# Optimization experiments

Measured on AMD Instinct MI355X. Metric: run time of the kernel, lower is better.

The kernel has to match this reference:

```python
import jax, jax.numpy as jnp
import numpy as np

NQ = 4      # n_qubits
NL = 1      # n_layers
IN_DIM = 512
HIDDEN = 256
B = 131072


def _apply_1q(state, gate, q, batched):
    """Apply a single-qubit gate on qubit q. state: [B, 2**NQ] complex.
    gate: [2,2] (shared) or [B,2,2] (per-sample)."""
    Bsz = state.shape[0]
    left, right = 2 ** q, 2 ** (NQ - q - 1)
    s = state.reshape(Bsz, left, 2, right)
    if batched:
        s = jnp.einsum('bij,bljr->blir', gate, s)
    else:
        s = jnp.einsum('ij,bljr->blir', gate, s)
    return s.reshape(Bsz, -1)


def _cnot_adjacent(state, q):
    """CNOT with control q, target q+1 (adjacent wires only)."""
    Bsz = state.shape[0]
    left, right = 2 ** q, 2 ** (NQ - q - 2)
    s = state.reshape(Bsz, left, 2, 2, right)
    # control=0 branch unchanged; control=1 branch has target flipped
    s = jnp.stack([s[:, :, 0], s[:, :, 1, ::-1]], axis=2)
    return s.reshape(Bsz, -1)


def _rot_gate(phi, theta, omega):
    """PennyLane Rot(phi,theta,omega) = RZ(omega) RY(theta) RZ(phi)."""
    c, s = jnp.cos(theta / 2), jnp.sin(theta / 2)
    ep = jnp.exp(-0.5j * (phi + omega).astype(jnp.complex64))
    em = jnp.exp(-0.5j * (phi - omega).astype(jnp.complex64))
    return jnp.array([[1.0, 0.0], [0.0, 0.0]], jnp.complex64) * (ep * c) + \
           jnp.array([[0.0, -1.0], [0.0, 0.0]], jnp.complex64) * (jnp.conj(em) * s) + \
           jnp.array([[0.0, 0.0], [1.0, 0.0]], jnp.complex64) * (em * s) + \
           jnp.array([[0.0, 0.0], [0.0, 1.0]], jnp.complex64) * (jnp.conj(ep) * c)


def quantum_circuit(angles, weights):
    """Batched statevector simulation. angles: [B, NQ] float, weights: [NL, NQ, 3].
    Returns PauliZ expectations per qubit: [B, NQ] float32."""
    Bsz = angles.shape[0]
    state = jnp.zeros((Bsz, 2 ** NQ), jnp.complex64).at[:, 0].set(1.0)
    # Angle embedding: RY(inputs[i]) on wire i
    for q in range(NQ):
        th = angles[:, q] / 2
        c, sn = jnp.cos(th), jnp.sin(th)
        g = jnp.stack([jnp.stack([c, -sn], -1), jnp.stack([sn, c], -1)], -2).astype(jnp.complex64)  # [B,2,2]
        state = _apply_1q(state, g, q, batched=True)
    # Entangling layers
    for l in range(NL):
        for q in range(NQ):
            g = _rot_gate(weights[l, q, 0], weights[l, q, 1], weights[l, q, 2])
            state = _apply_1q(state, g, q, batched=False)
        for q in range(NQ - 1):
            state = _cnot_adjacent(state, q)
    # <Z_q> = p(q=0) - p(q=1)
    probs = (jnp.abs(state) ** 2).reshape((Bsz,) + (2,) * NQ)
    outs = []
    for q in range(NQ):
        pq = jnp.moveaxis(probs, 1 + q, -1).reshape(Bsz, -1, 2).sum(1)
        outs.append(pq[:, 0] - pq[:, 1])
    return jnp.stack(outs, -1).astype(jnp.float32)


def setup_inputs() -> dict:
    key = jax.random.key(0)
    ks = jax.random.split(key, 10)
    sc1 = 1.0 / np.sqrt(IN_DIM)
    sch = 1.0 / np.sqrt(HIDDEN)
    scq = 1.0 / np.sqrt(NQ)
    return {
        'x': jax.random.normal(ks[0], (B, IN_DIM), jnp.float32),
        'W1': jax.random.uniform(ks[1], (IN_DIM, HIDDEN), jnp.float32, -sc1, sc1),
        'b1': jax.random.uniform(ks[2], (HIDDEN,), jnp.float32, -sc1, sc1),
        'qparams': jax.random.normal(ks[3], (NL, NQ, 3), jnp.float32),
        'Wr': jax.random.uniform(ks[4], (NQ, HIDDEN), jnp.float32, -scq, scq),
        'br': jax.random.uniform(ks[5], (HIDDEN,), jnp.float32, -scq, scq),
        'W2': jax.random.uniform(ks[6], (HIDDEN, HIDDEN), jnp.float32, -sch, sch),
        'b2': jax.random.uniform(ks[7], (HIDDEN,), jnp.float32, -sch, sch),
        'W3': jax.random.uniform(ks[8], (HIDDEN, HIDDEN), jnp.float32, -sch, sch),
        'b3': jax.random.uniform(ks[9], (HIDDEN,), jnp.float32, -sch, sch),
    }


def reference(x, W1, b1, qparams, Wr, br, W2, b2, W3, b3):
    # Linear -> ReLU -> (Dropout: identity in eval)
    h = jax.nn.relu(x @ W1 + b1)                       # [B, HIDDEN]
    # QuantumLinear: circuit uses first NQ features as RY angles, then readout
    q = quantum_circuit(h[:, :NQ], qparams)            # [B, NQ]
    h = jax.nn.relu(q @ Wr + br)                       # [B, HIDDEN]
    # depth-2 = 1 extra hidden block
    h = jax.nn.relu(h @ W2 + b2)
    return h @ W3 + b3                                 # [B, HIDDEN]
```

## Files before the change

### kernel.cpp

```cpp
#include <hip/hip_runtime.h>

typedef float  f32x4  __attribute__((ext_vector_type(4)));
typedef short  short8 __attribute__((ext_vector_type(8)));

#define BM   32
#define LPAD 264

__device__ __forceinline__ unsigned short f2bf(float f){
  union { float f; unsigned int u; } v; v.f = f;
  unsigned int u = v.u;
  return (unsigned short)((u + 0x7FFFu + ((u >> 16) & 1u)) >> 16);
}
__device__ __forceinline__ float bf2f(unsigned short h){
  union { unsigned int u; float f; } v; v.u = ((unsigned int)h) << 16;
  return v.f;
}

__global__ __launch_bounds__(256) void prep_kernel(
    const float* __restrict__ W1, const float* __restrict__ W2,
    const float* __restrict__ W3, float* __restrict__ w1c,
    unsigned short* __restrict__ W2H,
    unsigned short* __restrict__ W3H, unsigned short* __restrict__ W3L)
{
  int t = blockIdx.x * 256 + threadIdx.x;
  if (t < 2048) {
    w1c[t] = W1[(t >> 2) * 256 + (t & 3)];
  } else if (t < 2048 + 65536) {
    int f = t - 2048;
    int j = f & 7, lane = (f >> 3) & 63, ks = (f >> 9) & 7, n16 = f >> 12;
    int k = ks * 32 + (lane >> 4) * 8 + j;
    int n = n16 * 16 + (lane & 15);
    W2H[f] = f2bf(W2[k * 256 + n]);
  } else if (t < 2048 + 2 * 65536) {
    int f = t - 2048 - 65536;
    int j = f & 7, lane = (f >> 3) & 63, ks = (f >> 9) & 7, n16 = f >> 12;
    int k = ks * 32 + (lane >> 4) * 8 + j;
    int n = n16 * 16 + (lane & 15);
    float wv = W3[k * 256 + n];
    unsigned short hi = f2bf(wv);
    W3H[f] = hi;
    W3L[f] = f2bf(wv - bf2f(hi));
  }
}

__global__ __launch_bounds__(256) void angle_kernel(
    const float* __restrict__ x, const float* __restrict__ b1,
    const float* __restrict__ qp, const float* __restrict__ w1c,
    float* __restrict__ z)
{
  const int row = blockIdx.x * 256 + threadIdx.x;
  const f32x4* xr = (const f32x4*)(x + (size_t)row * 512);
  const f32x4* w1 = (const f32x4*)w1c;
  f32x4 p = {0.f, 0.f, 0.f, 0.f};
  #pragma unroll 8
  for (int i = 0; i < 128; i++) {
    f32x4 xa = xr[i];
    p += xa[0] * w1[4 * i + 0];
    p += xa[1] * w1[4 * i + 1];
    p += xa[2] * w1[4 * i + 2];
    p += xa[3] * w1[4 * i + 3];
  }
  float a0 = fmaxf(p[0] + b1[0], 0.f);
  float a1 = fmaxf(p[1] + b1[1], 0.f);
  float a2 = fmaxf(p[2] + b1[2], 0.f);
  float a3 = fmaxf(p[3] + b1[3], 0.f);

  float g00r[4], g00i[4], g01r[4], g01i[4], g10r[4], g10i[4], g11r[4], g11i[4];
  #pragma unroll
  for (int q = 0; q < 4; q++) {
    float phi = qp[q * 3 + 0], th = qp[q * 3 + 1], om = qp[q * 3 + 2];
    float c = cosf(0.5f * th), s = sinf(0.5f * th);
    float A1 = 0.5f * (phi + om), A2 = 0.5f * (phi - om);
    float c1 = cosf(A1), s1 = sinf(A1), c2 = cosf(A2), s2 = sinf(A2);
    g00r[q] =  c * c1;  g00i[q] = -c * s1;
    g01r[q] = -s * c2;  g01i[q] = -s * s2;
    g10r[q] =  s * c2;  g10i[q] = -s * s2;
    g11r[q] =  c * c1;  g11i[q] =  c * s1;
  }
  float cr0 = cosf(0.5f * a0), sv0 = sinf(0.5f * a0);
  float cr1 = cosf(0.5f * a1), sv1 = sinf(0.5f * a1);
  float cr2 = cosf(0.5f * a2), sv2 = sinf(0.5f * a2);
  float cr3 = cosf(0.5f * a3), sv3 = sinf(0.5f * a3);
  float sr[16], si[16];
  #pragma unroll
  for (int i = 0; i < 16; i++) {
    float v = ((i & 8) ? sv0 : cr0) * ((i & 4) ? sv1 : cr1) *
              ((i & 2) ? sv2 : cr2) * ((i & 1) ? sv3 : cr3);
    sr[i] = v; si[i] = 0.f;
  }
  #pragma unroll
  for (int q = 0; q < 4; q++) {
    const int st = 8 >> q;
    #pragma unroll
    for (int i = 0; i < 16; i++) {
      if (i & st) continue;
      const int i1 = i + st;
      float xr_ = sr[i], xi_ = si[i], yr_ = sr[i1], yi_ = si[i1];
      sr[i]  = g00r[q] * xr_ - g00i[q] * xi_ + g01r[q] * yr_ - g01i[q] * yi_;
      si[i]  = g00r[q] * xi_ + g00i[q] * xr_ + g01r[q] * yi_ + g01i[q] * yr_;
      sr[i1] = g10r[q] * xr_ - g10i[q] * xi_ + g11r[q] * yr_ - g11i[q] * yi_;
      si[i1] = g10r[q] * xi_ + g10i[q] * xr_ + g11r[q] * yi_ + g11i[q] * yr_;
    }
  }
  #pragma unroll
  for (int q = 0; q < 3; q++) {
    const int cb = 8 >> q, tb = 4 >> q;
    #pragma unroll
    for (int i = 0; i < 16; i++) {
      if ((i & cb) && !(i & tb)) {
        const int j = i | tb;
        float t1 = sr[i]; sr[i] = sr[j]; sr[j] = t1;
        float t2 = si[i]; si[i] = si[j]; si[j] = t2;
      }
    }
  }
  float z0 = 0.f, z1 = 0.f, z2 = 0.f, z3 = 0.f;
  #pragma unroll
  for (int i = 0; i < 16; i++) {
    float pb = sr[i] * sr[i] + si[i] * si[i];
    z0 += (i & 8) ? -pb : pb;
    z1 += (i & 4) ? -pb : pb;
    z2 += (i & 2) ? -pb : pb;
    z3 += (i & 1) ? -pb : pb;
  }
  f32x4 zv = {z0, z1, z2, z3};
  ((f32x4*)z)[row] = zv;
}

__global__ __launch_bounds__(256, 4) void mlp_kernel(
    const float* __restrict__ z,  const float* __restrict__ Wr,
    const float* __restrict__ br, const float* __restrict__ b2,
    const float* __restrict__ b3,
    const unsigned short* __restrict__ W2H,
    const unsigned short* __restrict__ W3H, const unsigned short* __restrict__ W3L,
    float* __restrict__ out)
{
  __shared__ __align__(16) char smem[512 + 2 * BM * LPAD * 2];
  f32x4* zl = (f32x4*)smem;
  unsigned short* a_hi = (unsigned short*)(smem + 512);
  unsigned short* a_lo = (unsigned short*)(smem + 512 + BM * LPAD * 2);
  float* fstage = (float*)(smem + 512);

  const int tid = threadIdx.x;
  const int w = tid >> 6, lane = tid & 63;
  const int l15 = lane & 15, l4 = lane >> 4;
  const int row0 = blockIdx.x * BM;

  if (tid < BM) zl[tid] = ((const f32x4*)z)[row0 + tid];
  __syncthreads();

  {
    float wr0 = Wr[tid], wr1 = Wr[256 + tid], wr2 = Wr[512 + tid], wr3 = Wr[768 + tid];
    float brv = br[tid];
    #pragma unroll 4
    for (int r = 0; r < BM; r++) {
      f32x4 zz = zl[r];
      float hv = fmaf(zz[0], wr0, fmaf(zz[1], wr1, fmaf(zz[2], wr2, fmaf(zz[3], wr3, brv))));
      hv = fmaxf(hv, 0.f);
      unsigned short hi = f2bf(hv);
      a_hi[r * LPAD + tid] = hi;
      a_lo[r * LPAD + tid] = f2bf(hv - bf2f(hi));
    }
  }
  __syncthreads();

  f32x4 acc[2][4];
  #pragma unroll
  for (int m = 0; m < 2; m++)
    #pragma unroll
    for (int n = 0; n < 4; n++) acc[m][n] = 0.f;
  #pragma unroll
  for (int ks = 0; ks < 8; ks++) {
    short8 ah[2], al[2];
    #pragma unroll
    for (int m = 0; m < 2; m++) {
      ah[m] = *(const short8*)&a_hi[(m * 16 + l15) * LPAD + ks * 32 + l4 * 8];
      al[m] = *(const short8*)&a_lo[(m * 16 + l15) * LPAD + ks * 32 + l4 * 8];
    }
    #pragma unroll
    for (int nf = 0; nf < 4; nf++) {
      short8 bh = *(const short8*)&W2H[(size_t)(((w * 4 + nf) * 8 + ks) * 64 + lane) * 8];
      #pragma unroll
      for (int m = 0; m < 2; m++) {
        acc[m][nf] = __builtin_amdgcn_mfma_f32_16x16x32_bf16(ah[m], bh, acc[m][nf], 0, 0, 0);
        acc[m][nf] = __builtin_amdgcn_mfma_f32_16x16x32_bf16(al[m], bh, acc[m][nf], 0, 0, 0);
      }
    }
  }
  __syncthreads();

  #pragma unroll
  for (int nf = 0; nf < 4; nf++) {
    int col = w * 64 + nf * 16 + l15;
    float b2v = b2[col];
    #pragma unroll
    for (int m = 0; m < 2; m++)
      #pragma unroll
      for (int i = 0; i < 4; i++) {
        float hv = fmaxf(acc[m][nf][i] + b2v, 0.f);
        unsigned short hi = f2bf(hv);
        int idx = (m * 16 + l4 * 4 + i) * LPAD + col;
        a_hi[idx] = hi;
        a_lo[idx] = f2bf(hv - bf2f(hi));
      }
  }
  __syncthreads();

  #pragma unroll
  for (int m = 0; m < 2; m++)
    #pragma unroll
    for (int n = 0; n < 4; n++) acc[m][n] = 0.f;
  #pragma unroll
  for (int ks = 0; ks < 8; ks++) {
    short8 ah[2], al[2];
    #pragma unroll
    for (int m = 0; m < 2; m++) {
      ah[m] = *(const short8*)&a_hi[(m * 16 + l15) * LPAD + ks * 32 + l4 * 8];
      al[m] = *(const short8*)&a_lo[(m * 16 + l15) * LPAD + ks * 32 + l4 * 8];
    }
    #pragma unroll
    for (int nf = 0; nf < 4; nf++) {
      size_t boff = (size_t)(((w * 4 + nf) * 8 + ks) * 64 + lane) * 8;
      short8 bh = *(const short8*)&W3H[boff];
      short8 bl = *(const short8*)&W3L[boff];
      #pragma unroll
      for (int m = 0; m < 2; m++) {
        acc[m][nf] = __builtin_amdgcn_mfma_f32_16x16x32_bf16(ah[m], bh, acc[m][nf], 0, 0, 0);
        acc[m][nf] = __builtin_amdgcn_mfma_f32_16x16x32_bf16(al[m], bh, acc[m][nf], 0, 0, 0);
        acc[m][nf] = __builtin_amdgcn_mfma_f32_16x16x32_bf16(ah[m], bl, acc[m][nf], 0, 0, 0);
      }
    }
  }
  __syncthreads();

  #pragma unroll
  for (int nf = 0; nf < 4; nf++) {
    int col = w * 64 + nf * 16 + l15;
    float b3v = b3[col];
    #pragma unroll
    for (int m = 0; m < 2; m++)
      #pragma unroll
      for (int i = 0; i < 4; i++)
        fstage[(m * 16 + l4 * 4 + i) * 260 + col] = acc[m][nf][i] + b3v;
  }
  __syncthreads();
  #pragma unroll
  for (int rr = 0; rr < 8; rr++) {
    int row = w * 8 + rr;
    f32x4 v = ((const f32x4*)&fstage[row * 260])[lane];
    ((f32x4*)(out + (size_t)(row0 + row) * 256))[lane] = v;
  }
}

extern "C" void kernel_launch(void* const* d_in, const int* in_sizes, int n_in,
                              void* d_out, int out_size, void* d_ws, size_t ws_size,
                              hipStream_t stream)
{
  const float* x  = (const float*)d_in[0];
  const float* W1 = (const float*)d_in[1];
  const float* b1 = (const float*)d_in[2];
  const float* qp = (const float*)d_in[3];
  const float* Wr = (const float*)d_in[4];
  const float* br = (const float*)d_in[5];
  const float* W2 = (const float*)d_in[6];
  const float* b2 = (const float*)d_in[7];
  const float* W3 = (const float*)d_in[8];
  const float* b3 = (const float*)d_in[9];
  float* out = (float*)d_out;

  char* ws = (char*)d_ws;
  float* w1c          = (float*)ws;
  unsigned short* W2H = (unsigned short*)(ws + 8192);
  unsigned short* W3H = (unsigned short*)(ws + 8192 + 1 * 131072);
  unsigned short* W3L = (unsigned short*)(ws + 8192 + 2 * 131072);
  float* z            = (float*)(ws + 8192 + 3 * 131072);

  prep_kernel<<<520, 256, 0, stream>>>(W1, W2, W3, w1c, W2H, W3H, W3L);
  angle_kernel<<<512, 256, 0, stream>>>(x, b1, qp, w1c, z);
  mlp_kernel<<<4096, 256, 0, stream>>>(z, Wr, br, b2, b3, W2H, W3H, W3L, out);
}
```

Before: 166.8 us.

## Fuse angle computation and circuit simulation into the MLP kernel

Removes the separate angle kernel and its global z buffer. Each MLP block now computes the first-layer projection for its 32 rows, with one wave per row using coalesced x loads and a shuffle reduction. It then runs the 4-qubit simulation on 8 lanes per wave and writes the results straight to shared memory. This saves a launch and a global round trip, but the serial circuit work now sits in front of the MFMA stage in every block and uses only 8 of 64 lanes, which may raise register pressure.

```diff
diff --git a/kernel.cpp b/kernel.cpp
--- a/kernel.cpp
+++ b/kernel.cpp
@@ -43,94 +43,11 @@
   }
 }
 
-__global__ __launch_bounds__(256) void angle_kernel(
-    const float* __restrict__ x, const float* __restrict__ b1,
+__global__ __launch_bounds__(256, 4) void qmlp_kernel(
+    const float* __restrict__ x,  const float* __restrict__ b1,
     const float* __restrict__ qp, const float* __restrict__ w1c,
-    float* __restrict__ z)
-{
-  const int row = blockIdx.x * 256 + threadIdx.x;
-  const f32x4* xr = (const f32x4*)(x + (size_t)row * 512);
-  const f32x4* w1 = (const f32x4*)w1c;
-  f32x4 p = {0.f, 0.f, 0.f, 0.f};
-  #pragma unroll 8
-  for (int i = 0; i < 128; i++) {
-    f32x4 xa = xr[i];
-    p += xa[0] * w1[4 * i + 0];
-    p += xa[1] * w1[4 * i + 1];
-    p += xa[2] * w1[4 * i + 2];
-    p += xa[3] * w1[4 * i + 3];
-  }
-  float a0 = fmaxf(p[0] + b1[0], 0.f);
-  float a1 = fmaxf(p[1] + b1[1], 0.f);
-  float a2 = fmaxf(p[2] + b1[2], 0.f);
-  float a3 = fmaxf(p[3] + b1[3], 0.f);
-
-  float g00r[4], g00i[4], g01r[4], g01i[4], g10r[4], g10i[4], g11r[4], g11i[4];
-  #pragma unroll
-  for (int q = 0; q < 4; q++) {
-    float phi = qp[q * 3 + 0], th = qp[q * 3 + 1], om = qp[q * 3 + 2];
-    float c = cosf(0.5f * th), s = sinf(0.5f * th);
-    float A1 = 0.5f * (phi + om), A2 = 0.5f * (phi - om);
-    float c1 = cosf(A1), s1 = sinf(A1), c2 = cosf(A2), s2 = sinf(A2);
-    g00r[q] =  c * c1;  g00i[q] = -c * s1;
-    g01r[q] = -s * c2;  g01i[q] = -s * s2;
-    g10r[q] =  s * c2;  g10i[q] = -s * s2;
-    g11r[q] =  c * c1;  g11i[q] =  c * s1;
-  }
-  float cr0 = cosf(0.5f * a0), sv0 = sinf(0.5f * a0);
-  float cr1 = cosf(0.5f * a1), sv1 = sinf(0.5f * a1);
-  float cr2 = cosf(0.5f * a2), sv2 = sinf(0.5f * a2);
-  float cr3 = cosf(0.5f * a3), sv3 = sinf(0.5f * a3);
-  float sr[16], si[16];
-  #pragma unroll
-  for (int i = 0; i < 16; i++) {
-    float v = ((i & 8) ? sv0 : cr0) * ((i & 4) ? sv1 : cr1) *
-              ((i & 2) ? sv2 : cr2) * ((i & 1) ? sv3 : cr3);
-    sr[i] = v; si[i] = 0.f;
-  }
-  #pragma unroll
-  for (int q = 0; q < 4; q++) {
-    const int st = 8 >> q;
-    #pragma unroll
-    for (int i = 0; i < 16; i++) {
-      if (i & st) continue;
-      const int i1 = i + st;
-      float xr_ = sr[i], xi_ = si[i], yr_ = sr[i1], yi_ = si[i1];
-      sr[i]  = g00r[q] * xr_ - g00i[q] * xi_ + g01r[q] * yr_ - g01i[q] * yi_;
-      si[i]  = g00r[q] * xi_ + g00i[q] * xr_ + g01r[q] * yi_ + g01i[q] * yr_;
-      sr[i1] = g10r[q] * xr_ - g10i[q] * xi_ + g11r[q] * yr_ - g11i[q] * yi_;
-      si[i1] = g10r[q] * xi_ + g10i[q] * xr_ + g11r[q] * yi_ + g11i[q] * yr_;
-    }
-  }
-  #pragma unroll
-  for (int q = 0; q < 3; q++) {
-    const int cb = 8 >> q, tb = 4 >> q;
-    #pragma unroll
-    for (int i = 0; i < 16; i++) {
-      if ((i & cb) && !(i & tb)) {
-        const int j = i | tb;
-        float t1 = sr[i]; sr[i] = sr[j]; sr[j] = t1;
-        float t2 = si[i]; si[i] = si[j]; si[j] = t2;
-      }
-    }
-  }
-  float z0 = 0.f, z1 = 0.f, z2 = 0.f, z3 = 0.f;
-  #pragma unroll
-  for (int i = 0; i < 16; i++) {
-    float pb = sr[i] * sr[i] + si[i] * si[i];
-    z0 += (i & 8) ? -pb : pb;
-    z1 += (i & 4) ? -pb : pb;
-    z2 += (i & 2) ? -pb : pb;
-    z3 += (i & 1) ? -pb : pb;
-  }
-  f32x4 zv = {z0, z1, z2, z3};
-  ((f32x4*)z)[row] = zv;
-}
-
-__global__ __launch_bounds__(256, 4) void mlp_kernel(
-    const float* __restrict__ z,  const float* __restrict__ Wr,
-    const float* __restrict__ br, const float* __restrict__ b2,
-    const float* __restrict__ b3,
+    const float* __restrict__ Wr, const float* __restrict__ br,
+    const float* __restrict__ b2, const float* __restrict__ b3,
     const unsigned short* __restrict__ W2H,
     const unsigned short* __restrict__ W3H, const unsigned short* __restrict__ W3L,
     float* __restrict__ out)
@@ -146,20 +63,112 @@
   const int l15 = lane & 15, l4 = lane >> 4;
   const int row0 = blockIdx.x * BM;
 
-  if (tid < BM) zl[tid] = ((const f32x4*)z)[row0 + tid];
+  f32x4 wc[8];
+  {
+    const f32x4* w1c4 = (const f32x4*)w1c;
+    #pragma unroll
+    for (int e = 0; e < 8; e++) wc[e] = w1c4[lane * 8 + e];
+  }
+  const f32x4 b1v = *(const f32x4*)b1;
+  float a0 = 0.f, a1 = 0.f, a2 = 0.f, a3 = 0.f;
+  #pragma unroll 2
+  for (int rr = 0; rr < 8; rr++) {
+    int grow = row0 + w * 8 + rr;
+    const f32x4* xr = (const f32x4*)(x + (size_t)grow * 512) + lane * 2;
+    f32x4 xa = xr[0], xb = xr[1];
+    f32x4 p = xa[0] * wc[0];
+    p += xa[1] * wc[1];  p += xa[2] * wc[2];  p += xa[3] * wc[3];
+    p += xb[0] * wc[4];  p += xb[1] * wc[5];  p += xb[2] * wc[6];  p += xb[3] * wc[7];
+    #pragma unroll
+    for (int off = 32; off > 0; off >>= 1) {
+      p[0] += __shfl_xor(p[0], off);
+      p[1] += __shfl_xor(p[1], off);
+      p[2] += __shfl_xor(p[2], off);
+      p[3] += __shfl_xor(p[3], off);
+    }
+    if (lane == rr) {
+      a0 = fmaxf(p[0] + b1v[0], 0.f);
+      a1 = fmaxf(p[1] + b1v[1], 0.f);
+      a2 = fmaxf(p[2] + b1v[2], 0.f);
+      a3 = fmaxf(p[3] + b1v[3], 0.f);
+    }
+  }
+
+  if (lane < 8) {
+    float g00r[4], g00i[4], g01r[4], g01i[4], g10r[4], g10i[4], g11r[4], g11i[4];
+    #pragma unroll
+    for (int q = 0; q < 4; q++) {
+      float phi = qp[q * 3 + 0], th = qp[q * 3 + 1], om = qp[q * 3 + 2];
+      float c = cosf(0.5f * th), s = sinf(0.5f * th);
+      float A1 = 0.5f * (phi + om), A2 = 0.5f * (phi - om);
+      float c1 = cosf(A1), s1 = sinf(A1), c2 = cosf(A2), s2 = sinf(A2);
+      g00r[q] =  c * c1;  g00i[q] = -c * s1;
+      g01r[q] = -s * c2;  g01i[q] = -s * s2;
+      g10r[q] =  s * c2;  g10i[q] = -s * s2;
+      g11r[q] =  c * c1;  g11i[q] =  c * s1;
+    }
+    float cr0 = cosf(0.5f * a0), sv0 = sinf(0.5f * a0);
+    float cr1 = cosf(0.5f * a1), sv1 = sinf(0.5f * a1);
+    float cr2 = cosf(0.5f * a2), sv2 = sinf(0.5f * a2);
+    float cr3 = cosf(0.5f * a3), sv3 = sinf(0.5f * a3);
+    float sr[16], si[16];
+    #pragma unroll
+    for (int i = 0; i < 16; i++) {
+      float v = ((i & 8) ? sv0 : cr0) * ((i & 4) ? sv1 : cr1) *
+                ((i & 2) ? sv2 : cr2) * ((i & 1) ? sv3 : cr3);
+      sr[i] = v; si[i] = 0.f;
+    }
+    #pragma unroll
+    for (int q = 0; q < 4; q++) {
+      const int st = 8 >> q;
+      #pragma unroll
+      for (int i = 0; i < 16; i++) {
+        if (i & st) continue;
+        const int i1 = i + st;
+        float xr_ = sr[i], xi_ = si[i], yr_ = sr[i1], yi_ = si[i1];
+        sr[i]  = g00r[q] * xr_ - g00i[q] * xi_ + g01r[q] * yr_ - g01i[q] * yi_;
+        si[i]  = g00r[q] * xi_ + g00i[q] * xr_ + g01r[q] * yi_ + g01i[q] * yr_;
+        sr[i1] = g10r[q] * xr_ - g10i[q] * xi_ + g11r[q] * yr_ - g11i[q] * yi_;
+        si[i1] = g10r[q] * xi_ + g10i[q] * xr_ + g11r[q] * yi_ + g11i[q] * yr_;
+      }
+    }
+    #pragma unroll
+    for (int q = 0; q < 3; q++) {
+      const int cb = 8 >> q, tb = 4 >> q;
+      #pragma unroll
+      for (int i = 0; i < 16; i++) {
+        if ((i & cb) && !(i & tb)) {
+          const int j = i | tb;
+          float t1 = sr[i]; sr[i] = sr[j]; sr[j] = t1;
+          float t2 = si[i]; si[i] = si[j]; si[j] = t2;
+        }
+      }
+    }
+    float z0 = 0.f, z1 = 0.f, z2 = 0.f, z3 = 0.f;
+    #pragma unroll
+    for (int i = 0; i < 16; i++) {
+      float pb = sr[i] * sr[i] + si[i] * si[i];
+      z0 += (i & 8) ? -pb : pb;
+      z1 += (i & 4) ? -pb : pb;
+      z2 += (i & 2) ? -pb : pb;
+      z3 += (i & 1) ? -pb : pb;
+    }
+    f32x4 zv = {z0, z1, z2, z3};
+    zl[w * 8 + lane] = zv;
+  }
   __syncthreads();
 
   {
     float wr0 = Wr[tid], wr1 = Wr[256 + tid], wr2 = Wr[512 + tid], wr3 = Wr[768 + tid];
     float brv = br[tid];
     #pragma unroll 4
-    for (int r = 0; r < BM; r++) {
-      f32x4 zz = zl[r];
+    for (int rr = 0; rr < BM; rr++) {
+      f32x4 zz = zl[rr];
       float hv = fmaf(zz[0], wr0, fmaf(zz[1], wr1, fmaf(zz[2], wr2, fmaf(zz[3], wr3, brv))));
       hv = fmaxf(hv, 0.f);
       unsigned short hi = f2bf(hv);
-      a_hi[r * LPAD + tid] = hi;
-      a_lo[r * LPAD + tid] = f2bf(hv - bf2f(hi));
+      a_hi[rr * LPAD + tid] = hi;
+      a_lo[rr * LPAD + tid] = f2bf(hv - bf2f(hi));
     }
   }
   __syncthreads();
@@ -273,9 +282,8 @@
   unsigned short* W2H = (unsigned short*)(ws + 8192);
   unsigned short* W3H = (unsigned short*)(ws + 8192 + 1 * 131072);
   unsigned short* W3L = (unsigned short*)(ws + 8192 + 2 * 131072);
-  float* z            = (float*)(ws + 8192 + 3 * 131072);
 
   prep_kernel<<<520, 256, 0, stream>>>(W1, W2, W3, w1c, W2H, W3H, W3L);
-  angle_kernel<<<512, 256, 0, stream>>>(x, b1, qp, w1c, z);
-  mlp_kernel<<<4096, 256, 0, stream>>>(z, Wr, br, b2, b3, W2H, W3H, W3L, out);
-}
+  qmlp_kernel<<<4096, 256, 0, stream>>>(x, b1, qp, w1c, Wr, br, b2, b3,
+                                        W2H, W3H, W3L, out);
+}
```

Result: slower. 181.4 us (+8.8%).

## Split angle dot product across four lanes and drop W3 low-bf16 correction

Applied to the files above, without the earlier changes.

The angle kernel now gives each row to four threads. Each thread reduces a quarter of the 512-wide dot product, and the partial sums are combined with cross-lane shuffles, giving four times more threads to hide the latency of streaming x. Separately, the low-order bf16 part of W3 is no longer built or used, which removes one MFMA per tile and one weight load in the final GEMM. The cost is lower precision in the output layer, and each group of four lanes now computes the full quantum circuit redundantly.

```diff
diff --git a/kernel.cpp b/kernel.cpp
--- a/kernel.cpp
+++ b/kernel.cpp
@@ -19,8 +19,7 @@
 __global__ __launch_bounds__(256) void prep_kernel(
     const float* __restrict__ W1, const float* __restrict__ W2,
     const float* __restrict__ W3, float* __restrict__ w1c,
-    unsigned short* __restrict__ W2H,
-    unsigned short* __restrict__ W3H, unsigned short* __restrict__ W3L)
+    unsigned short* __restrict__ W2H, unsigned short* __restrict__ W3H)
 {
   int t = blockIdx.x * 256 + threadIdx.x;
   if (t < 2048) {
@@ -36,10 +35,7 @@
     int j = f & 7, lane = (f >> 3) & 63, ks = (f >> 9) & 7, n16 = f >> 12;
     int k = ks * 32 + (lane >> 4) * 8 + j;
     int n = n16 * 16 + (lane & 15);
-    float wv = W3[k * 256 + n];
-    unsigned short hi = f2bf(wv);
-    W3H[f] = hi;
-    W3L[f] = f2bf(wv - bf2f(hi));
+    W3H[f] = f2bf(W3[k * 256 + n]);
   }
 }
 
@@ -48,18 +44,26 @@
     const float* __restrict__ qp, const float* __restrict__ w1c,
     float* __restrict__ z)
 {
-  const int row = blockIdx.x * 256 + threadIdx.x;
-  const f32x4* xr = (const f32x4*)(x + (size_t)row * 512);
-  const f32x4* w1 = (const f32x4*)w1c;
+  const int t = blockIdx.x * 256 + threadIdx.x;
+  const int row = t >> 2, c = t & 3;
+  const f32x4* xr = (const f32x4*)(x + (size_t)row * 512) + c * 32;
+  const f32x4* w1 = (const f32x4*)w1c + c * 128;
   f32x4 p = {0.f, 0.f, 0.f, 0.f};
   #pragma unroll 8
-  for (int i = 0; i < 128; i++) {
+  for (int i = 0; i < 32; i++) {
     f32x4 xa = xr[i];
     p += xa[0] * w1[4 * i + 0];
     p += xa[1] * w1[4 * i + 1];
     p += xa[2] * w1[4 * i + 2];
     p += xa[3] * w1[4 * i + 3];
   }
+  #pragma unroll
+  for (int off = 1; off < 4; off <<= 1) {
+    p[0] += __shfl_xor(p[0], off);
+    p[1] += __shfl_xor(p[1], off);
+    p[2] += __shfl_xor(p[2], off);
+    p[3] += __shfl_xor(p[3], off);
+  }
   float a0 = fmaxf(p[0] + b1[0], 0.f);
   float a1 = fmaxf(p[1] + b1[1], 0.f);
   float a2 = fmaxf(p[2] + b1[2], 0.f);
@@ -69,13 +73,13 @@
   #pragma unroll
   for (int q = 0; q < 4; q++) {
     float phi = qp[q * 3 + 0], th = qp[q * 3 + 1], om = qp[q * 3 + 2];
-    float c = cosf(0.5f * th), s = sinf(0.5f * th);
+    float cg = cosf(0.5f * th), sg = sinf(0.5f * th);
     float A1 = 0.5f * (phi + om), A2 = 0.5f * (phi - om);
     float c1 = cosf(A1), s1 = sinf(A1), c2 = cosf(A2), s2 = sinf(A2);
-    g00r[q] =  c * c1;  g00i[q] = -c * s1;
-    g01r[q] = -s * c2;  g01i[q] = -s * s2;
-    g10r[q] =  s * c2;  g10i[q] = -s * s2;
-    g11r[q] =  c * c1;  g11i[q] =  c * s1;
+    g00r[q] =  cg * c1;  g00i[q] = -cg * s1;
+    g01r[q] = -sg * c2;  g01i[q] = -sg * s2;
+    g10r[q] =  sg * c2;  g10i[q] = -sg * s2;
+    g11r[q] =  cg * c1;  g11i[q] =  cg * s1;
   }
   float cr0 = cosf(0.5f * a0), sv0 = sinf(0.5f * a0);
   float cr1 = cosf(0.5f * a1), sv1 = sinf(0.5f * a1);
@@ -123,8 +127,10 @@
     z2 += (i & 2) ? -pb : pb;
     z3 += (i & 1) ? -pb : pb;
   }
-  f32x4 zv = {z0, z1, z2, z3};
-  ((f32x4*)z)[row] = zv;
+  if (c == 0) {
+    f32x4 zv = {z0, z1, z2, z3};
+    ((f32x4*)z)[row] = zv;
+  }
 }
 
 __global__ __launch_bounds__(256, 4) void mlp_kernel(
@@ -132,7 +138,7 @@
     const float* __restrict__ br, const float* __restrict__ b2,
     const float* __restrict__ b3,
     const unsigned short* __restrict__ W2H,
-    const unsigned short* __restrict__ W3H, const unsigned short* __restrict__ W3L,
+    const unsigned short* __restrict__ W3H,
     float* __restrict__ out)
 {
   __shared__ __align__(16) char smem[512 + 2 * BM * LPAD * 2];
@@ -153,13 +159,13 @@
     float wr0 = Wr[tid], wr1 = Wr[256 + tid], wr2 = Wr[512 + tid], wr3 = Wr[768 + tid];
     float brv = br[tid];
     #pragma unroll 4
-    for (int r = 0; r < BM; r++) {
-      f32x4 zz = zl[r];
+    for (int rr = 0; rr < BM; rr++) {
+      f32x4 zz = zl[rr];
       float hv = fmaf(zz[0], wr0, fmaf(zz[1], wr1, fmaf(zz[2], wr2, fmaf(zz[3], wr3, brv))));
       hv = fmaxf(hv, 0.f);
       unsigned short hi = f2bf(hv);
-      a_hi[r * LPAD + tid] = hi;
-      a_lo[r * LPAD + tid] = f2bf(hv - bf2f(hi));
+      a_hi[rr * LPAD + tid] = hi;
+      a_lo[rr * LPAD + tid] = f2bf(hv - bf2f(hi));
     }
   }
   __syncthreads();
@@ -220,14 +226,11 @@
     }
     #pragma unroll
     for (int nf = 0; nf < 4; nf++) {
-      size_t boff = (size_t)(((w * 4 + nf) * 8 + ks) * 64 + lane) * 8;
-      short8 bh = *(const short8*)&W3H[boff];
-      short8 bl = *(const short8*)&W3L[boff];
+      short8 bh = *(const short8*)&W3H[(size_t)(((w * 4 + nf) * 8 + ks) * 64 + lane) * 8];
       #pragma unroll
       for (int m = 0; m < 2; m++) {
         acc[m][nf] = __builtin_amdgcn_mfma_f32_16x16x32_bf16(ah[m], bh, acc[m][nf], 0, 0, 0);
         acc[m][nf] = __builtin_amdgcn_mfma_f32_16x16x32_bf16(al[m], bh, acc[m][nf], 0, 0, 0);
-        acc[m][nf] = __builtin_amdgcn_mfma_f32_16x16x32_bf16(ah[m], bl, acc[m][nf], 0, 0, 0);
       }
     }
   }
@@ -272,10 +275,9 @@
   float* w1c          = (float*)ws;
   unsigned short* W2H = (unsigned short*)(ws + 8192);
   unsigned short* W3H = (unsigned short*)(ws + 8192 + 1 * 131072);
-  unsigned short* W3L = (unsigned short*)(ws + 8192 + 2 * 131072);
-  float* z            = (float*)(ws + 8192 + 3 * 131072);
-
-  prep_kernel<<<520, 256, 0, stream>>>(W1, W2, W3, w1c, W2H, W3H, W3L);
-  angle_kernel<<<512, 256, 0, stream>>>(x, b1, qp, w1c, z);
-  mlp_kernel<<<4096, 256, 0, stream>>>(z, Wr, br, b2, b3, W2H, W3H, W3L, out);
-}
+  float* z            = (float*)(ws + 8192 + 2 * 131072);
+
+  prep_kernel<<<520, 256, 0, stream>>>(W1, W2, W3, w1c, W2H, W3H);
+  angle_kernel<<<2048, 256, 0, stream>>>(x, b1, qp, w1c, z);
+  mlp_kernel<<<4096, 256, 0, stream>>>(z, Wr, br, b2, b3, W2H, W3H, out);
+}
```

Measured after the change: 253.2 us. +51.8%, slower.
